# Optimization experiments

Hardware: AMD Instinct MI355X
Metric: run time of the kernel (lower is better)

## Reference

```python
import jax, jax.numpy as jnp
import numpy as np

N = 50000
E = 800000
IN_DIM = 128
HID = 128
OUT = 128
HEADS = 4
HD_HID = HID // HEADS   # 32
HD_OUT = OUT // HEADS   # 32
NEG_SLOPE = 0.2


def gat_layer(H, src, dst, W, a_src, a_dst, b, num_nodes):
    """Standard GAT layer with concatenated heads.
    H: [N, Fin]; W: [Fin, heads*hd]; a_src/a_dst: [heads, hd]; b: [heads*hd]."""
    heads, hd = a_src.shape
    h = (H @ W).reshape(num_nodes, heads, hd)            # [N, H, D]
    alpha_s = jnp.einsum('nhd,hd->nh', h, a_src)         # [N, H]
    alpha_d = jnp.einsum('nhd,hd->nh', h, a_dst)         # [N, H]
    logits = alpha_s[src] + alpha_d[dst]                 # [E, H]
    logits = jax.nn.leaky_relu(logits, NEG_SLOPE)
    # segment softmax over incoming edges of each destination node
    seg_max = jax.ops.segment_max(logits, dst, num_segments=num_nodes)
    seg_max = jnp.where(jnp.isfinite(seg_max), seg_max, 0.0)
    ex = jnp.exp(logits - seg_max[dst])                  # [E, H]
    denom = jax.ops.segment_sum(ex, dst, num_segments=num_nodes)  # [N, H]
    att = ex / jnp.maximum(denom, 1e-16)[dst]            # [E, H]
    msg = att[:, :, None] * h[src]                       # [E, H, D]
    out = jax.ops.segment_sum(msg, dst, num_segments=num_nodes)   # [N, H, D]
    return out.reshape(num_nodes, heads * hd) + b


def setup_inputs() -> dict:
    key = jax.random.key(0)
    ks = jax.random.split(key, 10)
    X_all = jax.random.normal(ks[0], (N, IN_DIM), dtype=jnp.float32)
    edge_index = jax.random.randint(ks[1], (2, E), 0, N, dtype=jnp.int64)
    s0 = 1.0 / np.sqrt(IN_DIM)
    s1 = 1.0 / np.sqrt(HID)
    W0 = jax.random.normal(ks[2], (IN_DIM, HEADS * HD_HID), dtype=jnp.float32) * s0
    a_src0 = jax.random.normal(ks[3], (HEADS, HD_HID), dtype=jnp.float32) * s1
    a_dst0 = jax.random.normal(ks[4], (HEADS, HD_HID), dtype=jnp.float32) * s1
    b0 = jnp.zeros((HEADS * HD_HID,), dtype=jnp.float32)
    W1 = jax.random.normal(ks[5], (HID, HEADS * HD_OUT), dtype=jnp.float32) * s1
    a_src1 = jax.random.normal(ks[6], (HEADS, HD_OUT), dtype=jnp.float32) * s1
    a_dst1 = jax.random.normal(ks[7], (HEADS, HD_OUT), dtype=jnp.float32) * s1
    b1 = jnp.zeros((HEADS * HD_OUT,), dtype=jnp.float32)
    return {"X_all": X_all, "edge_index": edge_index,
            "W0": W0, "a_src0": a_src0, "a_dst0": a_dst0, "b0": b0,
            "W1": W1, "a_src1": a_src1, "a_dst1": a_dst1, "b1": b1}


def reference(X_all, edge_index, W0, a_src0, a_dst0, b0, W1, a_src1, a_dst1, b1):
    src, dst = edge_index[0], edge_index[1]
    num_nodes = X_all.shape[0]
    # layer 1 + ELU (dropout is identity in eval mode)
    H = gat_layer(X_all, src, dst, W0, a_src0, a_dst0, b0, num_nodes)
    H = jax.nn.elu(H)
    # layer 2 + ELU
    H = gat_layer(H, src, dst, W1, a_src1, a_dst1, b1, num_nodes)
    H = jax.nn.elu(H)
    return H
```

## Files before the change

### kernel.cpp

```cpp
#include <hip/hip_runtime.h>
#include <math.h>
#include <float.h>

#define NNODES 50000
#define NEDGES 800000

#define KB    196
#define NPB   256
#define CAPB  4608
#define EPB   4096
#define NABLK ((NEDGES + EPB - 1) / EPB)

typedef __attribute__((ext_vector_type(4))) _Float16 half4;
typedef __attribute__((ext_vector_type(8))) _Float16 half8;
typedef __attribute__((ext_vector_type(4))) float f32x4;

__global__ __launch_bounds__(256) void bininit_kernel(int* __restrict__ bincur) {
    int t = threadIdx.x;
    if (t < KB) bincur[t] = t * CAPB;
}

__global__ __launch_bounds__(256) void binA_kernel(
    const int* __restrict__ src, const int* __restrict__ dst,
    int* __restrict__ bincur, unsigned* __restrict__ binned)
{
    __shared__ int lhist[KB];
    __shared__ int lstart[KB];
    __shared__ int lcur[KB];
    __shared__ int gbase[KB];
    __shared__ unsigned lbuf[EPB];
    __shared__ int wtot[4];

    int t = threadIdx.x;
    int e0 = blockIdx.x * EPB;
    int ecnt = NEDGES - e0; if (ecnt > EPB) ecnt = EPB;

    for (int b = t; b < KB; b += 256) lhist[b] = 0;
    __syncthreads();

    for (int idx = t; idx < ecnt; idx += 256)
        atomicAdd(&lhist[((unsigned)dst[e0 + idx]) >> 8], 1);
    __syncthreads();

    {
        int lane = t & 63, w = t >> 6;
        int v = (t < KB) ? lhist[t] : 0;
        int x = v;
#pragma unroll
        for (int off = 1; off < 64; off <<= 1) {
            int y = __shfl_up(x, off, 64);
            if (lane >= off) x += y;
        }
        if (lane == 63) wtot[w] = x;
        __syncthreads();
        int wpre = 0;
#pragma unroll
        for (int j = 0; j < 4; ++j) if (j < w) wpre += wtot[j];
        int ex = wpre + x - v;
        if (t < KB) { lstart[t] = ex; lcur[t] = ex; }
    }
    __syncthreads();

    if (t < KB) {
        int c = lhist[t];
        gbase[t] = c ? atomicAdd(&bincur[t], c) : 0;
    }
    __syncthreads();

    for (int idx = t; idx < ecnt; idx += 256) {
        unsigned d = (unsigned)dst[e0 + idx];
        unsigned s = (unsigned)src[e0 + idx];
        int pos = atomicAdd(&lcur[d >> 8], 1);
        lbuf[pos] = (d << 16) | s;
    }
    __syncthreads();

    for (int idx = t; idx < ecnt; idx += 256) {
        unsigned p = lbuf[idx];
        int b = p >> 24;
        binned[gbase[b] + (idx - lstart[b])] = p;
    }
}

__global__ __launch_bounds__(256) void binB_kernel(
    const unsigned* __restrict__ binned, const int* __restrict__ bincur,
    int* __restrict__ csr_src, int2* __restrict__ node_info)
{
    __shared__ int lhist[NPB];
    __shared__ int lcur[NPB];
    __shared__ int wtot[4];
    int k = blockIdx.x;
    int t = threadIdx.x;
    int base = k * CAPB;
    int cnt = bincur[k] - base;

    lhist[t] = 0;
    __syncthreads();

    for (int i = t; i < cnt; i += 256)
        atomicAdd(&lhist[(binned[base + i] >> 16) & 0xFF], 1);
    __syncthreads();

    int lane = t & 63, w = t >> 6;
    int v = lhist[t];
    int x = v;
#pragma unroll
    for (int off = 1; off < 64; off <<= 1) {
        int y = __shfl_up(x, off, 64);
        if (lane >= off) x += y;
    }
    if (lane == 63) wtot[w] = x;
    __syncthreads();
    int wpre = 0;
#pragma unroll
    for (int j = 0; j < 4; ++j) if (j < w) wpre += wtot[j];
    int ex = wpre + x - v;
    lcur[t] = ex;
    int node = k * NPB + t;
    if (node < NNODES) node_info[node] = make_int2(base + ex, v);
    __syncthreads();

    for (int i = t; i < cnt; i += 256) {
        unsigned p = binned[base + i];
        int ln = (p >> 16) & 0xFF;
        int pos = atomicAdd(&lcur[ln], 1);
        csr_src[base + pos] = (int)(p & 0xFFFFu);
    }
}

__global__ __launch_bounds__(256) void prepw_kernel(
    const float* __restrict__ W0, const float* __restrict__ W1,
    _Float16* __restrict__ W0t, _Float16* __restrict__ W1t)
{
    int idx = blockIdx.x * 256 + threadIdx.x;
    if (idx < 128 * 128) {
        int cc = idx >> 7, k = idx & 127;
        W0t[idx] = (_Float16)W0[k * 128 + cc];
        W1t[idx] = (_Float16)W1[k * 128 + cc];
    }
}

#define GP 136
template <bool F32IN>
__global__ __launch_bounds__(256) void gemm_mfma_kernel(
    const void* __restrict__ Ain, const _Float16* __restrict__ Wt,
    const float* __restrict__ avs, const float* __restrict__ avd,
    _Float16* __restrict__ Hh, float* __restrict__ alpha_s,
    float* __restrict__ alpha_d, int nrows)
{
    __shared__ _Float16 Xs[64 * GP];
    __shared__ _Float16 Ws[128 * GP];

    int t = threadIdx.x;
    int brow = blockIdx.x * 64;

    {
        int r = t >> 2, q = t & 3;
        int grow = brow + r;
        _Float16* d = Xs + r * GP + q * 32;
        if (F32IN) {
            const float* A32 = (const float*)Ain;
            float4 v[8];
#pragma unroll
            for (int j = 0; j < 8; ++j) v[j] = make_float4(0, 0, 0, 0);
            if (grow < nrows) {
                const float4* p = (const float4*)(A32 + (size_t)grow * 128 + q * 32);
#pragma unroll
                for (int j = 0; j < 8; ++j) v[j] = p[j];
            }
#pragma unroll
            for (int j = 0; j < 8; ++j) {
                half4 h = {(_Float16)v[j].x, (_Float16)v[j].y,
                           (_Float16)v[j].z, (_Float16)v[j].w};
                *(half4*)(d + j * 4) = h;
            }
        } else {
            const _Float16* A16 = (const _Float16*)Ain;
            half8 v0 = {}, v1 = {}, v2 = {}, v3 = {};
            if (grow < nrows) {
                const half8* p = (const half8*)(A16 + (size_t)grow * 128 + q * 32);
                v0 = p[0]; v1 = p[1]; v2 = p[2]; v3 = p[3];
            }
            *(half8*)(d + 0)  = v0; *(half8*)(d + 8)  = v1;
            *(half8*)(d + 16) = v2; *(half8*)(d + 24) = v3;
        }
    }
    {
        int wr = t >> 1, wh = t & 1;
        const half8* p = (const half8*)(Wt + wr * 128 + wh * 64);
        _Float16* d = Ws + wr * GP + wh * 64;
#pragma unroll
        for (int j = 0; j < 8; ++j) *(half8*)(d + j * 8) = p[j];
    }
    __syncthreads();

    int wv = t >> 6, l = t & 63;
    int lrow = l & 15;
    int lk8  = (l >> 4) * 8;

    f32x4 acc[8];
#pragma unroll
    for (int n = 0; n < 8; ++n) acc[n] = (f32x4){0.f, 0.f, 0.f, 0.f};

    const _Float16* xbase = Xs + (wv * 16 + lrow) * GP + lk8;
#pragma unroll
    for (int kk = 0; kk < 4; ++kk) {
        half8 a = *(const half8*)(xbase + kk * 32);
#pragma unroll
        for (int n = 0; n < 8; ++n) {
            half8 bf = *(const half8*)(Ws + (n * 16 + lrow) * GP + kk * 32 + lk8);
            acc[n] = __builtin_amdgcn_mfma_f32_16x16x32_f16(a, bf, acc[n], 0, 0, 0);
        }
    }

    int c = lrow;
    int g = l >> 4;
#pragma unroll
    for (int n = 0; n < 8; ++n) {
#pragma unroll
        for (int r = 0; r < 4; ++r) {
            int row = brow + wv * 16 + g * 4 + r;
            if (row < nrows)
                Hh[(size_t)row * 128 + n * 16 + c] = (_Float16)acc[n][r];
        }
    }
#pragma unroll
    for (int hd = 0; hd < 4; ++hd) {
        float as0 = avs[hd * 32 + c], as1 = avs[hd * 32 + 16 + c];
        float ad0 = avd[hd * 32 + c], ad1 = avd[hd * 32 + 16 + c];
#pragma unroll
        for (int r = 0; r < 4; ++r) {
            float ps = acc[2 * hd][r] * as0 + acc[2 * hd + 1][r] * as1;
            float pd = acc[2 * hd][r] * ad0 + acc[2 * hd + 1][r] * ad1;
            ps += __shfl_xor(ps, 1); ps += __shfl_xor(ps, 2);
            ps += __shfl_xor(ps, 4); ps += __shfl_xor(ps, 8);
            pd += __shfl_xor(pd, 1); pd += __shfl_xor(pd, 2);
            pd += __shfl_xor(pd, 4); pd += __shfl_xor(pd, 8);
            if (c == 0) {
                int row = brow + wv * 16 + g * 4 + r;
                if (row < nrows) {
                    alpha_s[row * 4 + hd] = ps;
                    alpha_d[row * 4 + hd] = pd;
                }
            }
        }
    }
}

template <bool F16OUT>
__global__ __launch_bounds__(256) void att_gather_kernel(
    const int* __restrict__ csr_src, const int2* __restrict__ node_info,
    const float* __restrict__ alpha_s, const float* __restrict__ alpha_d,
    const _Float16* __restrict__ hbuf, const float* __restrict__ b,
    float* __restrict__ out32, _Float16* __restrict__ out16)
{
    int node = blockIdx.x * 4 + (threadIdx.x >> 6);
    if (node >= NNODES) return;
    int lane = threadIdx.x & 63;
    int p  = lane >> 4;
    int ft = lane & 15;
    int f  = ft * 8;
    int hh = ft >> 2;
    int2 bi = node_info[node];
    int beg = bi.x, end = bi.x + bi.y;
    float ad = alpha_d[node * 4 + hh];

    float acc[8] = {0.f, 0.f, 0.f, 0.f, 0.f, 0.f, 0.f, 0.f};
    float den = 0.f;
    int i = beg + p;
    for (; i + 4 < end; i += 8) {
        int s0 = csr_src[i];
        int s1 = csr_src[i + 4];
        float l0 = alpha_s[s0 * 4 + hh] + ad;
        float l1 = alpha_s[s1 * 4 + hh] + ad;
        half8 h0 = *(const half8*)(hbuf + (size_t)s0 * 128 + f);
        half8 h1 = *(const half8*)(hbuf + (size_t)s1 * 128 + f);
        l0 = fmaxf(l0, 0.2f * l0);
        l1 = fmaxf(l1, 0.2f * l1);
        float e0 = __expf(l0);
        float e1 = __expf(l1);
        den += e0 + e1;
#pragma unroll
        for (int j = 0; j < 8; ++j) acc[j] = fmaf(e0, (float)h0[j], acc[j]);
#pragma unroll
        for (int j = 0; j < 8; ++j) acc[j] = fmaf(e1, (float)h1[j], acc[j]);
    }
    for (; i < end; i += 4) {
        int s0 = csr_src[i];
        float l0 = alpha_s[s0 * 4 + hh] + ad;
        half8 h0 = *(const half8*)(hbuf + (size_t)s0 * 128 + f);
        l0 = fmaxf(l0, 0.2f * l0);
        float e0 = __expf(l0);
        den += e0;
#pragma unroll
        for (int j = 0; j < 8; ++j) acc[j] = fmaf(e0, (float)h0[j], acc[j]);
    }

#pragma unroll
    for (int j = 0; j < 8; ++j) {
        acc[j] += __shfl_xor(acc[j], 16);
        acc[j] += __shfl_xor(acc[j], 32);
    }
    den += __shfl_xor(den, 16);
    den += __shfl_xor(den, 32);

    if (p == 0) {
        float rd = 1.f / fmaxf(den, 1e-16f);
        float4 bv0 = *(const float4*)(b + f);
        float4 bv1 = *(const float4*)(b + f + 4);
        float x[8];
        x[0] = acc[0] * rd + bv0.x; x[1] = acc[1] * rd + bv0.y;
        x[2] = acc[2] * rd + bv0.z; x[3] = acc[3] * rd + bv0.w;
        x[4] = acc[4] * rd + bv1.x; x[5] = acc[5] * rd + bv1.y;
        x[6] = acc[6] * rd + bv1.z; x[7] = acc[7] * rd + bv1.w;
#pragma unroll
        for (int j = 0; j < 8; ++j) x[j] = (x[j] > 0.f) ? x[j] : expm1f(x[j]);
        if (F16OUT) {
            half8 hv;
#pragma unroll
            for (int j = 0; j < 8; ++j) hv[j] = (_Float16)x[j];
            *(half8*)(out16 + (size_t)node * 128 + f) = hv;
        } else {
            *(float4*)(out32 + (size_t)node * 128 + f) =
                make_float4(x[0], x[1], x[2], x[3]);
            *(float4*)(out32 + (size_t)node * 128 + f + 4) =
                make_float4(x[4], x[5], x[6], x[7]);
        }
    }
}

extern "C" void kernel_launch(void* const* d_in, const int* in_sizes, int n_in,
                              void* d_out, int out_size, void* d_ws, size_t ws_size,
                              hipStream_t stream) {
    const float* X    = (const float*)d_in[0];
    const int*   ei   = (const int*)d_in[1];
    const float* W0   = (const float*)d_in[2];
    const float* as0  = (const float*)d_in[3];
    const float* ad0  = (const float*)d_in[4];
    const float* b0   = (const float*)d_in[5];
    const float* W1   = (const float*)d_in[6];
    const float* as1  = (const float*)d_in[7];
    const float* ad1  = (const float*)d_in[8];
    const float* b1   = (const float*)d_in[9];

    const int* srcp = ei;
    const int* dstp = ei + NEDGES;

    _Float16* h16  = (_Float16*)d_ws;
    _Float16* ho16 = h16 + 6400000;
    _Float16* W0t  = ho16 + 6400000;
    _Float16* W1t  = W0t + 16384;
    float* as_ = (float*)(W1t + 16384);
    float* ad_ = as_ + 200000;
    unsigned* binned = (unsigned*)(ad_ + 200000);
    int*  csr_src   = (int*)(binned + (KB + 1) * CAPB);
    int2* node_info = (int2*)(csr_src + KB * CAPB);
    int*  bincur    = (int*)(node_info + NNODES);

    bininit_kernel<<<1, 256, 0, stream>>>(bincur);
    binA_kernel<<<NABLK, 256, 0, stream>>>(srcp, dstp, bincur, binned);
    binB_kernel<<<KB, 256, 0, stream>>>(binned, bincur, csr_src, node_info);

    prepw_kernel<<<64, 256, 0, stream>>>(W0, W1, W0t, W1t);

    const int NODE_BLOCKS = (NNODES + 3) / 4;
    const int GEMM_BLOCKS = (NNODES + 63) / 64;

    gemm_mfma_kernel<true><<<GEMM_BLOCKS, 256, 0, stream>>>(
        X, W0t, as0, ad0, h16, as_, ad_, NNODES);
    att_gather_kernel<true><<<NODE_BLOCKS, 256, 0, stream>>>(
        csr_src, node_info, as_, ad_, h16, b0, nullptr, ho16);

    gemm_mfma_kernel<false><<<GEMM_BLOCKS, 256, 0, stream>>>(
        ho16, W1t, as1, ad1, h16, as_, ad_, NNODES);
    att_gather_kernel<false><<<NODE_BLOCKS, 256, 0, stream>>>(
        csr_src, node_info, as_, ad_, h16, b1, (float*)d_out, nullptr);
}
```

Before: 156.5 us.

## Store features head-major and split attention gather per head with 16-bit CSR indices

The hidden features move from node-major [N,128] to head-major [4][N,32] layout. The attention gather now runs one block per (node group, head), so each wave works on a single head with 16 edges processed in parallel. CSR source indices are stored as 16-bit values, halving index traffic. The aim is a smaller working set per head for better L2 locality during the random gathers, at the cost of reading the CSR and alpha arrays four times and issuing 4x more blocks.

After: 329.0 us. +110.2%, slower.

```diff
diff --git a/kernel.cpp b/kernel.cpp
--- a/kernel.cpp
+++ b/kernel.cpp
@@ -10,6 +10,7 @@
 #define CAPB  4608
 #define EPB   4096
 #define NABLK ((NEDGES + EPB - 1) / EPB)
+#define HSZ   (NNODES * 32)
 
 typedef __attribute__((ext_vector_type(4))) _Float16 half4;
 typedef __attribute__((ext_vector_type(8))) _Float16 half8;
@@ -84,7 +85,7 @@
 
 __global__ __launch_bounds__(256) void binB_kernel(
     const unsigned* __restrict__ binned, const int* __restrict__ bincur,
-    int* __restrict__ csr_src, int2* __restrict__ node_info)
+    unsigned short* __restrict__ csr_src, int2* __restrict__ node_info)
 {
     __shared__ int lhist[NPB];
     __shared__ int lcur[NPB];
@@ -124,7 +125,7 @@
         unsigned p = binned[base + i];
         int ln = (p >> 16) & 0xFF;
         int pos = atomicAdd(&lcur[ln], 1);
-        csr_src[base + pos] = (int)(p & 0xFFFFu);
+        csr_src[base + pos] = (unsigned short)(p & 0xFFFFu);
     }
 }
 
@@ -145,8 +146,8 @@
 __global__ __launch_bounds__(256) void gemm_mfma_kernel(
     const void* __restrict__ Ain, const _Float16* __restrict__ Wt,
     const float* __restrict__ avs, const float* __restrict__ avd,
-    _Float16* __restrict__ Hh, float* __restrict__ alpha_s,
-    float* __restrict__ alpha_d, int nrows)
+    _Float16* __restrict__ Hh,
+    float* __restrict__ alpha_s, float* __restrict__ alpha_d, int nrows)
 {
     __shared__ _Float16 Xs[64 * GP];
     __shared__ _Float16 Ws[128 * GP];
@@ -178,7 +179,7 @@
             const _Float16* A16 = (const _Float16*)Ain;
             half8 v0 = {}, v1 = {}, v2 = {}, v3 = {};
             if (grow < nrows) {
-                const half8* p = (const half8*)(A16 + (size_t)grow * 128 + q * 32);
+                const half8* p = (const half8*)(A16 + (size_t)q * HSZ + (size_t)grow * 32);
                 v0 = p[0]; v1 = p[1]; v2 = p[2]; v3 = p[3];
             }
             *(half8*)(d + 0)  = v0; *(half8*)(d + 8)  = v1;
@@ -217,11 +218,13 @@
     int g = l >> 4;
 #pragma unroll
     for (int n = 0; n < 8; ++n) {
+        int head = n >> 1;
+        int off  = (n & 1) * 16 + c;
 #pragma unroll
         for (int r = 0; r < 4; ++r) {
             int row = brow + wv * 16 + g * 4 + r;
             if (row < nrows)
-                Hh[(size_t)row * 128 + n * 16 + c] = (_Float16)acc[n][r];
+                Hh[(size_t)head * HSZ + (size_t)row * 32 + off] = (_Float16)acc[n][r];
         }
     }
 #pragma unroll
@@ -249,32 +252,35 @@
 
 template <bool F16OUT>
 __global__ __launch_bounds__(256) void att_gather_kernel(
-    const int* __restrict__ csr_src, const int2* __restrict__ node_info,
+    const unsigned short* __restrict__ csr_src, const int2* __restrict__ node_info,
     const float* __restrict__ alpha_s, const float* __restrict__ alpha_d,
-    const _Float16* __restrict__ hbuf, const float* __restrict__ b,
-    float* __restrict__ out32, _Float16* __restrict__ out16)
-{
-    int node = blockIdx.x * 4 + (threadIdx.x >> 6);
-    if (node >= NNODES) return;
+    const _Float16* __restrict__ hbuf,
+    const float* __restrict__ b,
+    float* __restrict__ out32,
+    _Float16* __restrict__ out16)
+{
+    int blk = blockIdx.x;
+    int hh  = blk & 3;
+    int node = (blk >> 2) * 4 + (threadIdx.x >> 6);
     int lane = threadIdx.x & 63;
-    int p  = lane >> 4;
-    int ft = lane & 15;
-    int f  = ft * 8;
-    int hh = ft >> 2;
+    int p   = lane >> 2;
+    int ftl = lane & 3;
+    int f   = ftl * 8;
     int2 bi = node_info[node];
     int beg = bi.x, end = bi.x + bi.y;
     float ad = alpha_d[node * 4 + hh];
+    const _Float16* hb = hbuf + (size_t)hh * HSZ;
 
     float acc[8] = {0.f, 0.f, 0.f, 0.f, 0.f, 0.f, 0.f, 0.f};
     float den = 0.f;
     int i = beg + p;
-    for (; i + 4 < end; i += 8) {
+    for (; i + 16 < end; i += 32) {
         int s0 = csr_src[i];
-        int s1 = csr_src[i + 4];
+        int s1 = csr_src[i + 16];
         float l0 = alpha_s[s0 * 4 + hh] + ad;
         float l1 = alpha_s[s1 * 4 + hh] + ad;
-        half8 h0 = *(const half8*)(hbuf + (size_t)s0 * 128 + f);
-        half8 h1 = *(const half8*)(hbuf + (size_t)s1 * 128 + f);
+        half8 h0 = *(const half8*)(hb + (size_t)s0 * 32 + f);
+        half8 h1 = *(const half8*)(hb + (size_t)s1 * 32 + f);
         l0 = fmaxf(l0, 0.2f * l0);
         l1 = fmaxf(l1, 0.2f * l1);
         float e0 = __expf(l0);
@@ -285,10 +291,10 @@
 #pragma unroll
         for (int j = 0; j < 8; ++j) acc[j] = fmaf(e1, (float)h1[j], acc[j]);
     }
-    for (; i < end; i += 4) {
+    if (i < end) {
         int s0 = csr_src[i];
         float l0 = alpha_s[s0 * 4 + hh] + ad;
-        half8 h0 = *(const half8*)(hbuf + (size_t)s0 * 128 + f);
+        half8 h0 = *(const half8*)(hb + (size_t)s0 * 32 + f);
         l0 = fmaxf(l0, 0.2f * l0);
         float e0 = __expf(l0);
         den += e0;
@@ -297,34 +303,30 @@
     }
 
 #pragma unroll
-    for (int j = 0; j < 8; ++j) {
-        acc[j] += __shfl_xor(acc[j], 16);
-        acc[j] += __shfl_xor(acc[j], 32);
-    }
-    den += __shfl_xor(den, 16);
-    den += __shfl_xor(den, 32);
+    for (int off = 4; off < 64; off <<= 1) {
+#pragma unroll
+        for (int j = 0; j < 8; ++j) acc[j] += __shfl_xor(acc[j], off);
+        den += __shfl_xor(den, off);
+    }
 
     if (p == 0) {
         float rd = 1.f / fmaxf(den, 1e-16f);
-        float4 bv0 = *(const float4*)(b + f);
-        float4 bv1 = *(const float4*)(b + f + 4);
+        const float* bp = b + hh * 32 + f;
         float x[8];
-        x[0] = acc[0] * rd + bv0.x; x[1] = acc[1] * rd + bv0.y;
-        x[2] = acc[2] * rd + bv0.z; x[3] = acc[3] * rd + bv0.w;
-        x[4] = acc[4] * rd + bv1.x; x[5] = acc[5] * rd + bv1.y;
-        x[6] = acc[6] * rd + bv1.z; x[7] = acc[7] * rd + bv1.w;
-#pragma unroll
-        for (int j = 0; j < 8; ++j) x[j] = (x[j] > 0.f) ? x[j] : expm1f(x[j]);
+#pragma unroll
+        for (int j = 0; j < 8; ++j) {
+            x[j] = acc[j] * rd + bp[j];
+            x[j] = (x[j] > 0.f) ? x[j] : expm1f(x[j]);
+        }
         if (F16OUT) {
             half8 hv;
 #pragma unroll
             for (int j = 0; j < 8; ++j) hv[j] = (_Float16)x[j];
-            *(half8*)(out16 + (size_t)node * 128 + f) = hv;
+            *(half8*)(out16 + (size_t)hh * HSZ + (size_t)node * 32 + f) = hv;
         } else {
-            *(float4*)(out32 + (size_t)node * 128 + f) =
-                make_float4(x[0], x[1], x[2], x[3]);
-            *(float4*)(out32 + (size_t)node * 128 + f + 4) =
-                make_float4(x[4], x[5], x[6], x[7]);
+            float* op = out32 + (size_t)node * 128 + hh * 32 + f;
+            *(float4*)op       = make_float4(x[0], x[1], x[2], x[3]);
+            *(float4*)(op + 4) = make_float4(x[4], x[5], x[6], x[7]);
         }
     }
 }
@@ -347,14 +349,14 @@
     const int* dstp = ei + NEDGES;
 
     _Float16* h16  = (_Float16*)d_ws;
-    _Float16* ho16 = h16 + 6400000;
-    _Float16* W0t  = ho16 + 6400000;
+    _Float16* ho16 = h16 + 4 * HSZ;
+    _Float16* W0t  = ho16 + 4 * HSZ;
     _Float16* W1t  = W0t + 16384;
     float* as_ = (float*)(W1t + 16384);
     float* ad_ = as_ + 200000;
     unsigned* binned = (unsigned*)(ad_ + 200000);
-    int*  csr_src   = (int*)(binned + (KB + 1) * CAPB);
-    int2* node_info = (int2*)(csr_src + KB * CAPB);
+    unsigned short* csr_src = (unsigned short*)(binned + (KB + 1) * CAPB);
+    int2* node_info = (int2*)(csr_src + ((KB * CAPB + 1) & ~1));
     int*  bincur    = (int*)(node_info + NNODES);
 
     bininit_kernel<<<1, 256, 0, stream>>>(bincur);
@@ -363,16 +365,16 @@
 
     prepw_kernel<<<64, 256, 0, stream>>>(W0, W1, W0t, W1t);
 
-    const int NODE_BLOCKS = (NNODES + 3) / 4;
+    const int ATT_BLOCKS  = (NNODES / 4) * 4;
     const int GEMM_BLOCKS = (NNODES + 63) / 64;
 
     gemm_mfma_kernel<true><<<GEMM_BLOCKS, 256, 0, stream>>>(
         X, W0t, as0, ad0, h16, as_, ad_, NNODES);
-    att_gather_kernel<true><<<NODE_BLOCKS, 256, 0, stream>>>(
+    att_gather_kernel<true><<<ATT_BLOCKS, 256, 0, stream>>>(
         csr_src, node_info, as_, ad_, h16, b0, nullptr, ho16);
 
     gemm_mfma_kernel<false><<<GEMM_BLOCKS, 256, 0, stream>>>(
         ho16, W1t, as1, ad1, h16, as_, ad_, NNODES);
-    att_gather_kernel<false><<<NODE_BLOCKS, 256, 0, stream>>>(
+    att_gather_kernel<false><<<ATT_BLOCKS, 256, 0, stream>>>(
         csr_src, node_info, as_, ad_, h16, b1, (float*)d_out, nullptr);
 }
```
